# Kernel tuning notes

Hardware: AMD Instinct MI355X
Metric: run time of the kernel (lower is better)

Reference implementation:

```python
import jax, jax.numpy as jnp
import numpy as np

DEPTH = 4
H1 = 64
H2 = 16
NF = 5
L = 10.0
K = 4
DIM = 3
N = 2048
NK = N // 4
FEAT = 1 + 2 * NF * DIM  # r scalar + Nf (cos,sin) pairs of dim components


def _tn(k, shape, std=0.01):
    return jax.random.truncated_normal(k, -2.0, 2.0, shape, jnp.float32) * std


def setup_inputs() -> dict:
    key = jax.random.key(0)
    ks = jax.random.split(key, 16)
    comb0 = 3 * DIM + 3 * FEAT   # combine width at depth 0
    combd = 3 * H1 + 3 * H2      # combine width at later depths
    return {
        "sx": jax.random.uniform(ks[0], (N, DIM), jnp.float32) * L,
        "kpoints": jax.random.normal(ks[1], (2 * NK, DIM), jnp.float32),
        "we0": _tn(ks[2], (comb0, H1)), "be0": jnp.zeros((H1,), jnp.float32),
        "we_rest": _tn(ks[3], (DEPTH - 1, combd, H1)), "be_rest": jnp.zeros((DEPTH - 1, H1), jnp.float32),
        "wee0": _tn(ks[4], (FEAT, H2)), "bee0": jnp.zeros((H2,), jnp.float32),
        "wee_rest": _tn(ks[5], (DEPTH - 2, H2, H2)), "bee_rest": jnp.zeros((DEPTH - 2, H2), jnp.float32),
        "wep0": _tn(ks[6], (FEAT, H2)), "bep0": jnp.zeros((H2,), jnp.float32),
        "wep_rest": _tn(ks[7], (DEPTH - 2, H2, H2)), "bep_rest": jnp.zeros((DEPTH - 2, H2), jnp.float32),
        "orb_w_re": _tn(ks[8], (H1, H1)), "orb_w_im": _tn(ks[9], (H1, H1)),
        "orb_b_re": jnp.zeros((H1,), jnp.float32), "orb_b_im": jnp.zeros((H1,), jnp.float32),
        "w_det": _tn(ks[10], (K, H1, H1)),
        "bf_w": _tn(ks[11], (H1, DIM)),
        "mlp_w1": _tn(ks[12], (DIM, H1)), "mlp_b1": jnp.zeros((H1,), jnp.float32),
        "mlp_w2": _tn(ks[13], (H1, K * (NK - 1))), "mlp_b2": jnp.zeros((K * (NK - 1),), jnp.float32),
    }


def _fourier(rij, r):
    # interleaved [r, cos1, sin1, ..., cosNf, sinNf] like the original
    feats = [r[..., None]]
    for k in range(1, NF + 1):
        ang = (2.0 * np.pi * k / L) * rij
        feats.append(jnp.cos(ang))
        feats.append(jnp.sin(ang))
    return jnp.concatenate(feats, axis=-1)


def _combine(e, ee, ep):
    mm = e.shape[0]
    h = mm // 2
    g1a = jnp.broadcast_to(jnp.mean(e[:h], 0, keepdims=True), e.shape)
    g1b = jnp.broadcast_to(jnp.mean(e[h:], 0, keepdims=True), e.shape)
    g2a = jnp.mean(ee[:h], axis=0)
    g2b = jnp.mean(ee[h:], axis=0)
    g3 = jnp.mean(ep, axis=1)
    return jnp.concatenate([e, g1a, g1b, g2a, g2b, g3], axis=1)


def _forward(sx, kpoints, we0, be0, we_rest, be_rest, wee0, bee0, wee_rest, bee_rest,
             wep0, bep0, wep_rest, bep_rest, orb_w_re, orb_w_im, orb_b_re, orb_b_im,
             w_det, bf_w, mlp_w1, mlp_b1, mlp_w2, mlp_b2):
    n, dim = sx.shape
    m, m2 = n // 2, n // 4
    s, x = sx[:m], sx[m:]
    e = jnp.broadcast_to(kpoints[0][None, :], (m, dim))
    # electron-electron pairwise features (m,m,FEAT)
    rij = x[:, None, :] - x[None, :, :]
    eye = jnp.eye(m, dtype=x.dtype)
    r = jnp.linalg.norm(jnp.sin(np.pi * rij / L) + eye[..., None], axis=-1) * (1.0 - eye) * (L / np.pi)
    ee = _fourier(rij, r)
    # electron-proton pairwise features (m,m,FEAT)
    rij = x[:, None, :] - s[None, :, :]
    r = jnp.linalg.norm(jnp.sin(np.pi * rij / L), axis=-1) * (L / np.pi)
    ep = _fourier(rij, r)
    for d in range(DEPTH - 1):
        f = _combine(e, ee, ep)
        We, be = (we0, be0) if d == 0 else (we_rest[d - 1], be_rest[d - 1])
        Wee, bee = (wee0, bee0) if d == 0 else (wee_rest[d - 1], bee_rest[d - 1])
        Wep, bep = (wep0, bep0) if d == 0 else (wep_rest[d - 1], bep_rest[d - 1])
        e_u = jnp.tanh(f @ We + be)
        ee_u = jnp.tanh(ee @ Wee + bee)
        ep_u = jnp.tanh(ep @ Wep + bep)
        e, ee, ep = (e_u + e, ee_u + ee, ep_u + ep) if d > 0 else (e_u, ee_u, ep_u)
    f = _combine(e, ee, ep)
    e = jnp.tanh(f @ we_rest[-1] + be_rest[-1]) + e
    # complex orbitals and geminal pairing matrix phi: (K, m2, m2)
    orb = e.astype(jnp.complex64) @ (orb_w_re + 1j * orb_w_im) + (orb_b_re + 1j * orb_b_im)
    phi = jnp.einsum('ia,kab,jb->kij', orb[:m2], w_det.astype(jnp.complex64), orb[m2:]) + 1.0
    # backflow coordinates and plane-wave determinant factors
    z = e @ bf_w + x
    nk = kpoints.shape[0] // 2
    norm = 1.0 / L ** (dim / 2)
    D_up = norm * jnp.exp(1j * jnp.einsum('kd,id->ki', kpoints[:nk], z[:m2]))  # (nk, m2)
    D_dn = norm * jnp.exp(1j * jnp.einsum('kd,id->ki', kpoints[nk:], z[m2:]))  # (nk, m2)
    h = jnp.tanh(kpoints[0] @ mlp_w1 + mlp_b1)
    fdet = jax.nn.softplus(h @ mlp_w2 + mlp_b2).reshape(K, nk - 1)
    fdet = jnp.concatenate([jnp.ones((K, 1), fdet.dtype), fdet], axis=1)  # (K, nk)
    D = jnp.einsum('ai,ka,aj->kij', D_up, fdet.astype(D_up.dtype), jnp.conj(D_dn))
    # logdet_matmul: stable log of signed sum of K determinants
    phase, logabs = jnp.linalg.slogdet(D * phi)
    maxl = jnp.max(logabs)
    det = jnp.sum(phase * jnp.exp(logabs - maxl))
    return jnp.log(jnp.abs(det)) + maxl + jnp.log(det / jnp.abs(det))


def reference(sx, kpoints, we0, be0, we_rest, be_rest, wee0, bee0, wee_rest, bee_rest,
              wep0, bep0, wep_rest, bep_rest, orb_w_re, orb_w_im, orb_b_re, orb_b_im,
              w_det, bf_w, mlp_w1, mlp_b1, mlp_w2, mlp_b2):
    return _forward(sx, kpoints, we0, be0, we_rest, be_rest, wee0, bee0, wee_rest, bee_rest,
                    wep0, bep0, wep_rest, bep_rest, orb_w_re, orb_w_im, orb_b_re, orb_b_im,
                    w_det, bf_w, mlp_w1, mlp_b1, mlp_w2, mlp_b2)
```

## Files before the change

kernel.cpp:

```cpp
#include <hip/hip_runtime.h>

typedef unsigned int uint;
typedef unsigned short ushort;

#define M1 1024
#define MH 512
#define PI_F 3.14159265358979323846f
#define LBOX 10.0f
#define NB 32

__device__ __forceinline__ float bf2f(ushort h){ return __uint_as_float(((uint)h)<<16); }
__device__ __forceinline__ ushort f2bf(float f){ uint u = __float_as_uint(f); uint r = (u + 0x7fffu + ((u>>16)&1u))>>16; return (ushort)r; }
__device__ __forceinline__ float ftanh(float x){ float e = __expf(2.f*x); return 1.f - 2.f/(e+1.f); }
__device__ __forceinline__ float2 cmul(float2 a, float2 b){ return make_float2(a.x*b.x - a.y*b.y, a.x*b.y + a.y*b.x); }
__device__ __forceinline__ void cfma(float2& c, float2 a, float2 b){
  c.x = fmaf(a.x,b.x,fmaf(-a.y,b.y,c.x));
  c.y = fmaf(a.x,b.y,fmaf(a.y,b.x,c.y));
}

__device__ __forceinline__ void fourier31(float d0, float d1, float d2, bool diag, float f[31]){
  const float k1 = PI_F / LBOX;
  float s[3], c[3];
  __sincosf(k1*d0, &s[0], &c[0]);
  __sincosf(k1*d1, &s[1], &c[1]);
  __sincosf(k1*d2, &s[2], &c[2]);
  float r = diag ? 0.f : (LBOX/PI_F)*sqrtf(s[0]*s[0]+s[1]*s[1]+s[2]*s[2]);
  f[0] = r;
  float cb[3], sb[3], cc[3], sc[3];
  #pragma unroll
  for (int d=0; d<3; ++d){ cb[d] = 1.f - 2.f*s[d]*s[d]; sb[d] = 2.f*s[d]*c[d]; cc[d]=cb[d]; sc[d]=sb[d]; }
  #pragma unroll
  for (int k=0;k<5;++k){
    #pragma unroll
    for (int d=0; d<3; ++d){ f[1+6*k+d] = cc[d]; f[4+6*k+d] = sc[d]; }
    if (k<4){
      #pragma unroll
      for (int d=0; d<3; ++d){
        float nc = cc[d]*cb[d]-sc[d]*sb[d];
        float ns = sc[d]*cb[d]+cc[d]*sb[d];
        cc[d]=nc; sc[d]=ns;
      }
    }
  }
}

__global__ void k_init(float* __restrict__ p, int n, int* __restrict__ rowmap){
  int i = blockIdx.x*256 + threadIdx.x;
  if (i < 2048) rowmap[i] = i & 511;
  for (int q=i; q<n; q+=gridDim.x*256) p[q] = 0.f;
}

__global__ __launch_bounds__(256) void k_pair0(const float* __restrict__ sx, const float* __restrict__ W,
                                               const float* __restrict__ b, ushort* __restrict__ out, int is_ee,
                                               float* __restrict__ gA, float* __restrict__ gB,
                                               float* __restrict__ gH){
  int bx = blockIdx.x;
  int i = bx >> 2;
  int chunk = bx & 3;
  int j = (chunk << 8) + threadIdx.x;
  const float* xs = sx + 3*M1;
  float xi0 = xs[3*i], xi1 = xs[3*i+1], xi2 = xs[3*i+2];
  const float* oth = is_ee ? xs : sx;
  float y0 = oth[3*j], y1 = oth[3*j+1], y2 = oth[3*j+2];
  float f[31];
  fourier31(xi0-y0, xi1-y1, xi2-y2, is_ee && (i==j), f);
  float acc[16];
  #pragma unroll
  for (int o=0;o<16;++o) acc[o] = b[o];
  #pragma unroll
  for (int c=0;c<31;++c){ float fv = f[c];
    #pragma unroll
    for (int o=0;o<16;++o) acc[o] = fmaf(fv, W[c*16+o], acc[o]);
  }
  float hv[16];
  #pragma unroll
  for (int o=0;o<16;++o) hv[o] = ftanh(acc[o]);
  uint u[8];
  #pragma unroll
  for (int h=0;h<8;++h){
    u[h] = (uint)f2bf(hv[2*h]) | ((uint)f2bf(hv[2*h+1])<<16);
  }
  uint4* dst = (uint4*)(out + ((size_t)i*M1 + j)*16);
  dst[0] = make_uint4(u[0],u[1],u[2],u[3]);
  dst[1] = make_uint4(u[4],u[5],u[6],u[7]);
  __shared__ float buf[256*49];
  #pragma unroll
  for (int c=0;c<31;++c) buf[threadIdx.x*49+c] = f[c];
  #pragma unroll
  for (int c=0;c<16;++c) buf[threadIdx.x*49+31+c] = hv[c];
  __syncthreads();
  #pragma unroll
  for (int s=128; s>0; s>>=1){
    if (threadIdx.x < s){
      #pragma unroll
      for (int c=0;c<47;++c) buf[threadIdx.x*49+c] += buf[(threadIdx.x+s)*49+c];
    }
    __syncthreads();
  }
  if (threadIdx.x < 31){
    float* g = (is_ee && chunk >= 2) ? gB : gA;
    atomicAdd(&g[i*31+threadIdx.x], buf[threadIdx.x]);
  } else if (threadIdx.x < 47 && gH){
    atomicAdd(&gH[i*16 + (threadIdx.x-31)], buf[threadIdx.x]);
  }
}

__global__ __launch_bounds__(256) void k_pairU(ushort* __restrict__ ten, const float* __restrict__ W,
                                               const float* __restrict__ b, float* __restrict__ gOut){
  size_t base = ((size_t)blockIdx.x*256 + threadIdx.x)*16;
  uint4 a0 = ((uint4*)(ten+base))[0];
  uint4 a1 = ((uint4*)(ten+base))[1];
  uint uu[8] = {a0.x,a0.y,a0.z,a0.w,a1.x,a1.y,a1.z,a1.w};
  float v[16];
  #pragma unroll
  for (int h=0;h<8;++h){ v[2*h] = bf2f((ushort)(uu[h]&0xffffu)); v[2*h+1] = bf2f((ushort)(uu[h]>>16)); }
  float acc[16];
  #pragma unroll
  for (int o=0;o<16;++o) acc[o] = b[o];
  #pragma unroll
  for (int c=0;c<16;++c){ float fv = v[c];
    #pragma unroll
    for (int o=0;o<16;++o) acc[o] = fmaf(fv, W[c*16+o], acc[o]);
  }
  float nv[16];
  #pragma unroll
  for (int o=0;o<16;++o) nv[o] = ftanh(acc[o]) + v[o];
  uint w[8];
  #pragma unroll
  for (int h=0;h<8;++h){
    w[h] = (uint)f2bf(nv[2*h]) | ((uint)f2bf(nv[2*h+1])<<16);
  }
  ((uint4*)(ten+base))[0] = make_uint4(w[0],w[1],w[2],w[3]);
  ((uint4*)(ten+base))[1] = make_uint4(w[4],w[5],w[6],w[7]);
  __shared__ float buf[256*17];
  if (gOut){
    #pragma unroll
    for (int c=0;c<16;++c) buf[threadIdx.x*17+c] = nv[c];
    __syncthreads();
    #pragma unroll
    for (int s=128; s>0; s>>=1){
      if (threadIdx.x < s){
        #pragma unroll
        for (int c=0;c<16;++c) buf[threadIdx.x*17+c] += buf[(threadIdx.x+s)*17+c];
      }
      __syncthreads();
    }
    if (threadIdx.x < 16){
      int i = blockIdx.x >> 2;
      atomicAdd(&gOut[i*16 + threadIdx.x], buf[threadIdx.x]);
    }
  }
}

__global__ __launch_bounds__(256) void k_gee(const ushort* __restrict__ ten, float* __restrict__ gA, float* __restrict__ gB){
  int jb = blockIdx.x >> 3;
  int ic = blockIdx.x & 7;
  int jl = threadIdx.x & 63;
  int iq = threadIdx.x >> 6;
  int j = jb*64 + jl;
  float acc[16];
  #pragma unroll
  for (int c=0;c<16;++c) acc[c]=0.f;
  for (int s=0;s<32;++s){
    int i = ic*128 + iq + 4*s;
    const uint4* src = (const uint4*)(ten + ((size_t)i*M1 + j)*16);
    uint4 a0 = src[0], a1 = src[1];
    uint uu[8]={a0.x,a0.y,a0.z,a0.w,a1.x,a1.y,a1.z,a1.w};
    #pragma unroll
    for (int h=0;h<8;++h){ acc[2*h]+=bf2f((ushort)(uu[h]&0xffffu)); acc[2*h+1]+=bf2f((ushort)(uu[h]>>16)); }
  }
  __shared__ float red[4][64][16];
  #pragma unroll
  for (int c=0;c<16;++c) red[iq][jl][c]=acc[c];
  __syncthreads();
  if (iq==0){
    float* out = (ic<4)? gA : gB;
    #pragma unroll
    for (int c=0;c<16;++c){
      float t = red[0][jl][c]+red[1][jl][c]+red[2][jl][c]+red[3][jl][c];
      atomicAdd(&out[j*16+c], t);
    }
  }
}

__global__ __launch_bounds__(256) void k_e0(const float* __restrict__ kp, const float* __restrict__ g2a,
    const float* __restrict__ g2b, const float* __restrict__ g3, const float* __restrict__ W,
    const float* __restrict__ b, float* __restrict__ eout, float* __restrict__ g1out){
  int p = blockIdx.x*4 + (threadIdx.x>>6);
  int o = threadIdx.x & 63;
  float acc = b[o];
  #pragma unroll
  for (int d=0; d<3; ++d){
    acc = fmaf(kp[d], W[d*64+o] + W[(d+3)*64+o] + W[(d+6)*64+o], acc);
  }
  const float i512 = 1.f/512.f, i1024 = 1.f/1024.f;
  #pragma unroll
  for (int c=0;c<31;++c){
    float sg = (c!=0 && ((c-1)%6)>=3) ? -i512 : i512;
    acc = fmaf(g2a[p*31+c]*sg, W[(9+c)*64+o], acc);
  }
  #pragma unroll
  for (int c=0;c<31;++c){
    float sg = (c!=0 && ((c-1)%6)>=3) ? -i512 : i512;
    acc = fmaf(g2b[p*31+c]*sg, W[(40+c)*64+o], acc);
  }
  #pragma unroll
  for (int c=0;c<31;++c) acc = fmaf(g3[p*31+c]*i1024, W[(71+c)*64+o], acc);
  float v = ftanh(acc);
  eout[p*64+o] = v;
  atomicAdd(&g1out[(p<MH?0:64)+o], v);
}

__global__ __launch_bounds__(256) void k_eupd(const float* __restrict__ eprev, float* __restrict__ eout,
    const float* __restrict__ W, const float* __restrict__ b, const float* __restrict__ g1in,
    const float* __restrict__ g2a, const float* __restrict__ g2b, const float* __restrict__ g3,
    float* __restrict__ g1out){
  int p = blockIdx.x*4 + (threadIdx.x>>6);
  int o = threadIdx.x & 63;
  const float i512 = 1.f/512.f, i1024 = 1.f/1024.f;
  float acc = b[o];
  #pragma unroll 8
  for (int c=0;c<64;++c) acc = fmaf(eprev[p*64+c], W[c*64+o], acc);
  #pragma unroll 8
  for (int c=0;c<64;++c) acc = fmaf(g1in[c]*i512, W[(64+c)*64+o], acc);
  #pragma unroll 8
  for (int c=0;c<64;++c) acc = fmaf(g1in[64+c]*i512, W[(128+c)*64+o], acc);
  #pragma unroll
  for (int c=0;c<16;++c) acc = fmaf(g2a[p*16+c]*i512, W[(192+c)*64+o], acc);
  #pragma unroll
  for (int c=0;c<16;++c) acc = fmaf(g2b[p*16+c]*i512, W[(208+c)*64+o], acc);
  #pragma unroll
  for (int c=0;c<16;++c) acc = fmaf(g3[p*16+c]*i1024, W[(224+c)*64+o], acc);
  float v = ftanh(acc) + eprev[p*64+o];
  eout[p*64+o] = v;
  if (g1out) atomicAdd(&g1out[(p<MH?0:64)+o], v);
}

__global__ __launch_bounds__(256) void k_orbz(const float* __restrict__ e4, const float* __restrict__ Wre,
    const float* __restrict__ Wim, const float* __restrict__ bre, const float* __restrict__ bim,
    const float* __restrict__ bfw, const float* __restrict__ sx, float* __restrict__ ore,
    float* __restrict__ oim, float* __restrict__ z){
  int p = blockIdx.x*4 + (threadIdx.x>>6);
  int o = threadIdx.x & 63;
  float ar = bre[o], ai = bim[o];
  #pragma unroll 8
  for (int a=0;a<64;++a){ float ev = e4[p*64+a]; ar = fmaf(ev, Wre[a*64+o], ar); ai = fmaf(ev, Wim[a*64+o], ai); }
  ore[p*64+o]=ar; oim[p*64+o]=ai;
  if (o<3){
    float zz = sx[(M1+p)*3+o];
    for (int a=0;a<64;++a) zz = fmaf(e4[p*64+a], bfw[a*3+o], zz);
    z[p*3+o]=zz;
  }
}

__global__ __launch_bounds__(256) void k_fdet(const float* __restrict__ kp, const float* __restrict__ w1,
    const float* __restrict__ b1, const float* __restrict__ w2, const float* __restrict__ b2,
    float* __restrict__ fdet){
  __shared__ float hs[64];
  int tid = threadIdx.x;
  if (tid < 64){
    float acc = b1[tid];
    for (int d=0;d<3;++d) acc = fmaf(kp[d], w1[d*64+tid], acc);
    hs[tid] = ftanh(acc);
  }
  __syncthreads();
  int c = blockIdx.x*256 + tid;
  if (c < 2044){
    float acc = b2[c];
    #pragma unroll 8
    for (int o=0;o<64;++o) acc = fmaf(hs[o], w2[o*2044+c], acc);
    float sp = (acc > 20.f) ? acc : log1pf(__expf(acc));
    int kk = c / 511, idx = c % 511;
    fdet[kk*512 + 1 + idx] = sp;
  }
  if (blockIdx.x == 0 && tid < 4) fdet[tid*512] = 1.f;
}

__global__ __launch_bounds__(256) void k_uv(const float* __restrict__ kp, const float* __restrict__ z,
                                            float2* __restrict__ U, float2* __restrict__ V){
  int gid = blockIdx.x*256 + threadIdx.x;
  int sel = gid >> 18;
  int rem = gid & 262143;
  int a = rem >> 9;
  int col = rem & 511;
  const float nrm = 0.031622776601683794f;
  const float* kr = kp + (sel ? (512+a)*3 : a*3);
  const float* zr = z + (sel ? (512+col)*3 : col*3);
  float th = kr[0]*zr[0] + kr[1]*zr[1] + kr[2]*zr[2];
  float s, c; __sincosf(th, &s, &c);
  float2 v = make_float2(nrm*c, nrm*s);
  if (sel) V[a*512+col] = v; else U[a*512+col] = v;
}

__global__ __launch_bounds__(256) void k_T(const float* __restrict__ ore, const float* __restrict__ oim,
                                           const float* __restrict__ wdet, float2* __restrict__ T){
  int k = blockIdx.x >> 7;
  int iblk = blockIdx.x & 127;
  int i = iblk*4 + (threadIdx.x>>6);
  int bc = threadIdx.x & 63;
  __shared__ float wd[4096];
  for (int t = threadIdx.x; t < 4096; t += 256) wd[t] = wdet[k*4096 + t];
  __syncthreads();
  float ar=0.f, ai=0.f;
  #pragma unroll 8
  for (int a=0;a<64;++a){
    float w = wd[a*64+bc];
    ar = fmaf(ore[i*64+a], w, ar);
    ai = fmaf(oim[i*64+a], w, ai);
  }
  T[((size_t)k*512 + i)*64 + bc] = make_float2(ar, ai);
}

__global__ __launch_bounds__(256) void k_M(const float2* __restrict__ U, const float2* __restrict__ V,
    const float* __restrict__ fdet, const float2* __restrict__ T, const float* __restrict__ ore,
    const float* __restrict__ oim, float2* __restrict__ Mb){
  __shared__ float2 As[16*66];
  __shared__ float2 Bs[16*66];
  int k = blockIdx.z;
  int ib = blockIdx.y * 64, jb = blockIdx.x * 64;
  int tid = threadIdx.x;
  int ti = (tid >> 4) * 4;
  int tj = (tid & 15) * 4;
  const float* fk = fdet + k*512;
  float2 acc[4][4];
  #pragma unroll
  for (int a=0;a<4;++a){
    #pragma unroll
    for (int b=0;b<4;++b) acc[a][b] = make_float2(0.f,0.f);
  }
  for (int a0=0; a0<512; a0+=16){
    #pragma unroll
    for (int s=0;s<4;++s){
      int t = tid + s*256;
      int aa = t >> 6, il = t & 63;
      int a = a0 + aa;
      float fv = fk[a];
      float2 u = U[a*512 + ib + il];
      As[aa*66+il] = make_float2(u.x*fv, u.y*fv);
      float2 v = V[a*512 + jb + il];
      Bs[aa*66+il] = make_float2(v.x, -v.y);
    }
    __syncthreads();
    #pragma unroll
    for (int aa=0;aa<16;++aa){
      float2 Av[4], Bv[4];
      #pragma unroll
      for (int q=0;q<4;++q){ Av[q] = As[aa*66+ti+q]; Bv[q] = Bs[aa*66+tj+q]; }
      #pragma unroll
      for (int qi=0;qi<4;++qi){
        #pragma unroll
        for (int qj=0;qj<4;++qj) cfma(acc[qi][qj], Av[qi], Bv[qj]);
      }
    }
    __syncthreads();
  }
  float2 ph[4][4];
  #pragma unroll
  for (int a=0;a<4;++a){
    #pragma unroll
    for (int b=0;b<4;++b) ph[a][b] = make_float2(1.f,0.f);
  }
  for (int b0=0; b0<64; b0+=16){
    #pragma unroll
    for (int s=0;s<4;++s){
      int t = tid + s*256;
      int aa = t >> 6, il = t & 63;
      As[aa*66+il] = T[((size_t)k*512 + ib + il)*64 + b0 + aa];
      int oidx = (512 + jb + il)*64 + b0 + aa;
      Bs[aa*66+il] = make_float2(ore[oidx], oim[oidx]);
    }
    __syncthreads();
    #pragma unroll
    for (int aa=0;aa<16;++aa){
      float2 Av[4], Bv[4];
      #pragma unroll
      for (int q=0;q<4;++q){ Av[q] = As[aa*66+ti+q]; Bv[q] = Bs[aa*66+tj+q]; }
      #pragma unroll
      for (int qi=0;qi<4;++qi){
        #pragma unroll
        for (int qj=0;qj<4;++qj) cfma(ph[qi][qj], Av[qi], Bv[qj]);
      }
    }
    __syncthreads();
  }
  #pragma unroll
  for (int qi=0;qi<4;++qi){
    size_t ro = ((size_t)k*512 + ib + ti + qi)*512 + jb + tj;
    #pragma unroll
    for (int qj=0;qj<4;++qj) Mb[ro+qj] = cmul(acc[qi][qj], ph[qi][qj]);
  }
}

__global__ __launch_bounds__(512)
void k_panel(float2* __restrict__ Mb, float2* __restrict__ LinvG,
             int* __restrict__ rowmap, int* __restrict__ swapc, int col0){
  int k = blockIdx.x;
  float2* Mk = Mb + (size_t)k*512*512;
  int R = 512 - col0;
  int R64 = R < 64 ? R : 64;
  int rl = threadIdx.x;
  bool active = rl < R;
  int wv = rl >> 6;
  __shared__ float2 mir[64*33];
  __shared__ float2 Us[NB*33];
  __shared__ float2 dinv[NB];
  __shared__ float2 Ls[NB*NB];
  __shared__ float2 Yv[NB*NB];
  __shared__ int winslot[NB];
  __shared__ int newposS[64];
  int rm_orig = active ? rowmap[k*512 + col0 + rl] : 0;
  float2 X[NB];
  if (rl >= 64 && active){
    const float4* rp = (const float4*)(Mk + (size_t)rm_orig*512 + col0);
    #pragma unroll
    for (int q=0;q<NB/2;++q){ float4 v = rp[q]; X[2*q]=make_float2(v.x,v.y); X[2*q+1]=make_float2(v.z,v.w); }
  }
  if (wv == 0){
    if (rl < R64){
      const float4* rp = (const float4*)(Mk + (size_t)rm_orig*512 + col0);
      #pragma unroll
      for (int q=0;q<NB/2;++q){
        float4 v = rp[q];
        mir[rl*33+2*q]   = make_float2(v.x,v.y);
        mir[rl*33+2*q+1] = make_float2(v.z,v.w);
      }
    }
    bool done = false;
    int winpos = 0;
    for (int cc=0; cc<NB; ++cc){
      bool cand = (rl < R64) && !done;
      float2 cv = make_float2(0.f,0.f);
      if (cand) cv = mir[rl*33+cc];
      float val = cand ? fmaf(cv.x,cv.x,cv.y*cv.y) : -1.f;
      int idx = rl;
      #pragma unroll
      for (int off=32; off>0; off>>=1){
        float ov = __shfl_xor(val, off);
        int   oi = __shfl_xor(idx, off);
        if (ov > val || (ov == val && oi < idx)){ val = ov; idx = oi; }
      }
      int p = idx;
      if (rl == 0) winslot[cc] = p;
      if (rl == p){ done = true; winpos = cc; }
      float2 dg = mir[p*33+cc];
      float dn = 1.f/fmaf(dg.x,dg.x,dg.y*dg.y);
      float2 inv = make_float2(dg.x*dn, -dg.y*dn);
      if (cand && rl != p){
        float2 l = cmul(cv, inv);
        mir[rl*33+cc] = l;
        for (int j=cc+1; j<NB; ++j){
          float2 pr = mir[p*33+j];
          float2 xv = mir[rl*33+j];
          xv.x = fmaf(-l.x, pr.x, fmaf( l.y, pr.y, xv.x));
          xv.y = fmaf(-l.x, pr.y, fmaf(-l.y, pr.x, xv.y));
          mir[rl*33+j] = xv;
        }
      }
    }
    unsigned long long nwmask = __ballot(rl < R64 && !done);
    int np = 0;
    if (rl < R64){
      np = done ? winpos : (NB + (int)__popcll(nwmask & ((1ull<<rl)-1ull)));
      newposS[rl] = np;
      rowmap[k*512 + col0 + np] = rm_orig;
      float4* wp = (float4*)(Mk + (size_t)rm_orig*512 + col0);
      #pragma unroll
      for (int q=0;q<NB/2;++q){
        float2 a = mir[rl*33+2*q], bq = mir[rl*33+2*q+1];
        wp[q] = make_float4(a.x,a.y,bq.x,bq.y);
      }
    }
    {
      int cnt = 0;
      for (int t=0;t<R64;++t){
        int nt = newposS[t];
        if (rl < R64 && t > rl && nt < np) cnt++;
      }
      #pragma unroll
      for (int off=32; off>0; off>>=1) cnt += __shfl_xor(cnt, off);
      if (rl == 0) swapc[k] += cnt;
    }
    if (rl < NB){
      int ws = winslot[rl];
      #pragma unroll
      for (int j=0;j<NB;++j){
        float2 v = mir[ws*33+j];
        Us[rl*33+j] = v;
        float2 lv;
        if      (j <  rl) lv = v;
        else if (j == rl) lv = make_float2(1.f,0.f);
        else              lv = make_float2(0.f,0.f);
        Ls[rl*NB+j] = lv;
      }
      float2 d = Us[rl*33+rl];
      float dn = 1.f/fmaf(d.x,d.x,d.y*d.y);
      dinv[rl] = make_float2(d.x*dn, -d.y*dn);
    }
  }
  __syncthreads();
  if (rl >= 64 && active){
    #pragma unroll
    for (int j=0;j<NB;++j){
      float2 t = X[j];
      #pragma unroll
      for (int q=0;q<NB;++q){
        if (q < j){
          float2 u = Us[q*33+j];
          t.x = fmaf(-X[q].x, u.x, fmaf( X[q].y, u.y, t.x));
          t.y = fmaf(-X[q].x, u.y, fmaf(-X[q].y, u.x, t.y));
        }
      }
      X[j] = cmul(t, dinv[j]);
    }
    float4* wp = (float4*)(Mk + (size_t)rm_orig*512 + col0);
    #pragma unroll
    for (int q=0;q<NB/2;++q) wp[q] = make_float4(X[2*q].x,X[2*q].y,X[2*q+1].x,X[2*q+1].y);
  }
  if (rl < NB){
    for (int i=0;i<NB;++i){
      float2 acc = (i==rl)? make_float2(1.f,0.f) : make_float2(0.f,0.f);
      for (int q=rl; q<i; ++q){
        float2 lv = Ls[i*NB+q];
        float2 yv = Yv[q*NB+rl];
        acc.x = fmaf(-lv.x, yv.x, fmaf( lv.y, yv.y, acc.x));
        acc.y = fmaf(-lv.x, yv.y, fmaf(-lv.y, yv.x, acc.y));
      }
      Yv[i*NB+rl] = acc;
    }
  }
  __syncthreads();
  {
    float4* dst = (float4*)(LinvG + (size_t)k*(NB*NB));
    const float4* src = (const float4*)Yv;
    for (int q=rl; q<NB*NB/2; q+=blockDim.x) dst[q] = src[q];
  }
}

__global__ __launch_bounds__(256) void k_gemm(float2* __restrict__ Mb, const float2* __restrict__ LinvG,
                                              const int* __restrict__ rowmap, int col0){
  int k = blockIdx.z;
  float2* Mk = Mb + (size_t)k*512*512;
  int e0 = col0 + NB;
  int r0 = e0 + blockIdx.x*32;
  int j0c = e0 + blockIdx.y*32;
  int tid = threadIdx.x;
  int jl = tid & 31, rg = tid >> 5;
  __shared__ float2 As[NB*33];
  __shared__ float2 Bs[NB*33];
  __shared__ float2 Av[NB*33];
  __shared__ float2 Li[NB*NB];
  __shared__ int prA[32];
  __shared__ int prB[NB];
  if (tid < 32) prA[tid] = rowmap[k*512 + r0 + tid];
  else if (tid < 64) prB[tid-32] = rowmap[k*512 + col0 + (tid-32)];
  {
    const float4* src = (const float4*)(LinvG + (size_t)k*(NB*NB));
    float4* dst = (float4*)Li;
    for (int q=tid; q<NB*NB/2; q+=256) dst[q] = src[q];
  }
  __syncthreads();
  #pragma unroll
  for (int s=0;s<4;++s){
    int a = rg + 8*s;
    Av[a*33 + jl] = Mk[(size_t)prB[a]*512 + j0c + jl];
  }
  for (int t=tid; t<1024; t+=256){
    int rl = t >> 5, kk = t & 31;
    As[kk*33+rl] = Mk[(size_t)prA[rl]*512 + col0 + kk];
  }
  __syncthreads();
  #pragma unroll
  for (int s=0;s<4;++s){
    int m = rg + 8*s;
    float2 acc = make_float2(0.f,0.f);
    #pragma unroll 8
    for (int a=0;a<NB;++a) cfma(acc, Li[m*NB+a], Av[a*33+jl]);
    Bs[m*33+jl] = acc;
  }
  __syncthreads();
  int i0 = (tid >> 4)*2, j0 = (tid & 15)*2;
  float2 a00={0,0},a01={0,0},a10={0,0},a11={0,0};
  #pragma unroll 16
  for (int kk=0;kk<NB;++kk){
    float2 A0 = As[kk*33+i0], A1 = As[kk*33+i0+1];
    float2 B0 = Bs[kk*33+j0], B1 = Bs[kk*33+j0+1];
    cfma(a00,A0,B0); cfma(a01,A0,B1); cfma(a10,A1,B0); cfma(a11,A1,B1);
  }
  size_t ro0 = (size_t)prA[i0]*512 + j0c + j0;
  size_t ro1 = (size_t)prA[i0+1]*512 + j0c + j0;
  float2 c0 = Mk[ro0];   c0.x-=a00.x; c0.y-=a00.y; Mk[ro0]=c0;
  float2 c1 = Mk[ro0+1]; c1.x-=a01.x; c1.y-=a01.y; Mk[ro0+1]=c1;
  float2 c2 = Mk[ro1];   c2.x-=a10.x; c2.y-=a10.y; Mk[ro1]=c2;
  float2 c3 = Mk[ro1+1]; c3.x-=a11.x; c3.y-=a11.y; Mk[ro1+1]=c3;
}

__global__ void k_det(const float2* __restrict__ Mb, const int* __restrict__ rowmap,
                      const int* __restrict__ swapc, float* __restrict__ out, int out_size){
  int tid = threadIdx.x;
  int k = tid >> 6, lane = tid & 63;
  const float2* Mk = Mb + (size_t)k*512*512;
  double la = 0.0, ang = 0.0;
  for (int q=0;q<8;++q){
    int i = lane*8 + q;
    int pr = rowmap[k*512 + i];
    float2 u = Mk[(size_t)pr*512+i];
    double re = (double)u.x, im = (double)u.y;
    la += 0.5*log(re*re + im*im);
    ang += atan2(im, re);
  }
  #pragma unroll
  for (int off=32; off>0; off>>=1){
    la += __shfl_down(la, off);
    ang += __shfl_down(ang, off);
  }
  __shared__ double las[4], angs[4];
  if (lane==0){
    las[k] = la;
    angs[k] = ang + 3.14159265358979323846*(double)(swapc[k] & 1);
  }
  __syncthreads();
  if (tid==0){
    double mx = las[0];
    for (int q=1;q<4;++q) mx = fmax(mx, las[q]);
    double sre=0.0, sim=0.0;
    for (int q=0;q<4;++q){
      double w = exp(las[q]-mx);
      sre += w*cos(angs[q]);
      sim += w*sin(angs[q]);
    }
    double mag = sqrt(sre*sre+sim*sim);
    out[0] = (float)(log(mag)+mx);
    if (out_size > 1) out[1] = (float)atan2(sim, sre);
    for (int q=2;q<out_size;++q) out[q] = 0.f;
  }
}

extern "C" void kernel_launch(void* const* d_in, const int* in_sizes, int n_in,
                              void* d_out, int out_size, void* d_ws, size_t ws_size,
                              hipStream_t stream){
  const float* sx   = (const float*)d_in[0];
  const float* kp   = (const float*)d_in[1];
  const float* we0  = (const float*)d_in[2];
  const float* be0  = (const float*)d_in[3];
  const float* weR  = (const float*)d_in[4];
  const float* beR  = (const float*)d_in[5];
  const float* wee0 = (const float*)d_in[6];
  const float* bee0 = (const float*)d_in[7];
  const float* weeR = (const float*)d_in[8];
  const float* beeR = (const float*)d_in[9];
  const float* wep0 = (const float*)d_in[10];
  const float* bep0 = (const float*)d_in[11];
  const float* wepR = (const float*)d_in[12];
  const float* bepR = (const float*)d_in[13];
  const float* owre = (const float*)d_in[14];
  const float* owim = (const float*)d_in[15];
  const float* obre = (const float*)d_in[16];
  const float* obim = (const float*)d_in[17];
  const float* wdet = (const float*)d_in[18];
  const float* bfw  = (const float*)d_in[19];
  const float* mw1  = (const float*)d_in[20];
  const float* mb1  = (const float*)d_in[21];
  const float* mw2  = (const float*)d_in[22];
  const float* mb2  = (const float*)d_in[23];

  char* ws = (char*)d_ws;
  size_t off = 0;
  auto alloc = [&](size_t bytes)->char*{
    char* p = ws + off;
    off = (off + bytes + 255) & ~(size_t)255;
    return p;
  };
  ushort* ee   = (ushort*)alloc(33554432);
  ushort* ep   = (ushort*)alloc(33554432);
  float2* Mb   = (float2*)alloc(8388608);
  float2* U    = (float2*)alloc(2097152);
  float2* V    = (float2*)alloc(2097152);
  float2* T    = (float2*)alloc(1048576);
  float*  eS   = (float*)alloc(1048576);
  float*  ore  = (float*)alloc(262144);
  float*  oim  = (float*)alloc(262144);
  float*  z    = (float*)alloc(12288);
  float*  fdet = (float*)alloc(8192);
  float2* Linv = (float2*)alloc(131072);
  int*    rowmap = (int*)alloc(8192);
  char*   zst  = ws + off;
  float*  g2a0 = (float*)alloc(126976);
  float*  g2b0 = (float*)alloc(126976);
  float*  g30  = (float*)alloc(126976);
  float*  geeA = (float*)alloc(196608);
  float*  geeB = (float*)alloc(196608);
  float*  gep  = (float*)alloc(196608);
  float*  g1s  = (float*)alloc(1536);
  int*    swpc = (int*)alloc(16);
  int zn = (int)(((char*)(swpc+4) - zst)/4);

  float* e1 = eS;           float* e2 = eS + 65536;
  float* e3 = eS + 131072;  float* e4 = eS + 196608;
  float* geeA1 = geeA;      float* geeA2 = geeA+16384; float* geeA3 = geeA+32768;
  float* geeB1 = geeB;      float* geeB2 = geeB+16384; float* geeB3 = geeB+32768;
  float* gep1  = gep;       float* gep2  = gep+16384;  float* gep3  = gep+32768;
  float* g1s1 = g1s; float* g1s2 = g1s+128; float* g1s3 = g1s+256;

  k_init<<<256,256,0,stream>>>((float*)zst, zn, rowmap);
  k_pair0<<<4096,256,0,stream>>>(sx, wee0, bee0, ee, 1, g2a0, g2b0, nullptr);
  k_pair0<<<4096,256,0,stream>>>(sx, wep0, bep0, ep, 0, g30, g30, gep1);
  k_e0<<<256,256,0,stream>>>(kp, g2a0, g2b0, g30, we0, be0, e1, g1s1);
  k_gee<<<128,256,0,stream>>>(ee, geeA1, geeB1);
  k_eupd<<<256,256,0,stream>>>(e1, e2, weR, beR, g1s1, geeA1, geeB1, gep1, g1s2);
  k_pairU<<<4096,256,0,stream>>>(ee, weeR, beeR, nullptr);
  k_pairU<<<4096,256,0,stream>>>(ep, wepR, bepR, gep2);
  k_gee<<<128,256,0,stream>>>(ee, geeA2, geeB2);
  k_eupd<<<256,256,0,stream>>>(e2, e3, weR+240*64, beR+64, g1s2, geeA2, geeB2, gep2, g1s3);
  k_pairU<<<4096,256,0,stream>>>(ee, weeR+256, beeR+16, nullptr);
  k_pairU<<<4096,256,0,stream>>>(ep, wepR+256, bepR+16, gep3);
  k_gee<<<128,256,0,stream>>>(ee, geeA3, geeB3);
  k_eupd<<<256,256,0,stream>>>(e3, e4, weR+2*240*64, beR+128, g1s3, geeA3, geeB3, gep3, nullptr);
  k_orbz<<<256,256,0,stream>>>(e4, owre, owim, obre, obim, bfw, sx, ore, oim, z);
  k_fdet<<<8,256,0,stream>>>(kp, mw1, mb1, mw2, mb2, fdet);
  k_uv<<<2048,256,0,stream>>>(kp, z, U, V);
  k_T<<<512,256,0,stream>>>(ore, oim, wdet, T);
  k_M<<<dim3(8,8,4),256,0,stream>>>(U, V, fdet, T, ore, oim, Mb);
  for (int tpan=0;tpan<16;++tpan){
    int col0 = tpan*NB;
    int R = 512 - col0;
    int Rpad = (R + 63) & ~63;
    k_panel<<<4, Rpad, 0, stream>>>(Mb, Linv, rowmap, swpc, col0);
    if (tpan < 15){
      int nch = 15 - tpan;
      k_gemm<<<dim3(nch,nch,4),256,0,stream>>>(Mb, Linv, rowmap, col0);
    }
  }
  k_det<<<1,256,0,stream>>>(Mb, rowmap, swpc, (float*)d_out, out_size);
  (void)in_sizes; (void)n_in; (void)ws_size;
}
```

Measured before the change: 1.894 ms.

## Retile k_M into 32x32 output tiles with 2x2 per-thread work

The M-matrix build kernel moves from 64x64 tiles with 4x4 outputs per thread over 256 blocks to 32x32 tiles with 2x2 outputs per thread over 1024 blocks. The phase GEMM now stages the full T and orbital slices into shared memory once instead of in four chunks. The aim is to fill more of the GPU's compute units on this small launch, at the cost of less register reuse and more global traffic per output.

```diff
diff --git a/kernel.cpp b/kernel.cpp
--- a/kernel.cpp
+++ b/kernel.cpp
@@ -314,81 +314,57 @@
 __global__ __launch_bounds__(256) void k_M(const float2* __restrict__ U, const float2* __restrict__ V,
     const float* __restrict__ fdet, const float2* __restrict__ T, const float* __restrict__ ore,
     const float* __restrict__ oim, float2* __restrict__ Mb){
-  __shared__ float2 As[16*66];
-  __shared__ float2 Bs[16*66];
-  int k = blockIdx.z;
-  int ib = blockIdx.y * 64, jb = blockIdx.x * 64;
-  int tid = threadIdx.x;
-  int ti = (tid >> 4) * 4;
-  int tj = (tid & 15) * 4;
+  __shared__ float2 sm[4160];
+  int k = blockIdx.x >> 8;
+  int ty = (blockIdx.x >> 4) & 15;
+  int tx = blockIdx.x & 15;
+  int ib = ty*32, jb = tx*32;
+  int i0 = (threadIdx.x >> 4)*2;
+  int j0 = threadIdx.x & 15;
   const float* fk = fdet + k*512;
-  float2 acc[4][4];
-  #pragma unroll
-  for (int a=0;a<4;++a){
-    #pragma unroll
-    for (int b=0;b<4;++b) acc[a][b] = make_float2(0.f,0.f);
-  }
+  float2 a00={0,0},a01={0,0},a10={0,0},a11={0,0};
+  float2* As = sm;
+  float2* Bs = sm + 512;
   for (int a0=0; a0<512; a0+=16){
-    #pragma unroll
-    for (int s=0;s<4;++s){
-      int t = tid + s*256;
-      int aa = t >> 6, il = t & 63;
+    for (int t = threadIdx.x; t < 512; t += 256){
+      int aa = t >> 5, il = t & 31;
       int a = a0 + aa;
       float fv = fk[a];
       float2 u = U[a*512 + ib + il];
-      As[aa*66+il] = make_float2(u.x*fv, u.y*fv);
+      As[t] = make_float2(u.x*fv, u.y*fv);
       float2 v = V[a*512 + jb + il];
-      Bs[aa*66+il] = make_float2(v.x, -v.y);
+      Bs[t] = make_float2(v.x, -v.y);
     }
     __syncthreads();
     #pragma unroll
-    for (int aa=0;aa<16;++aa){
-      float2 Av[4], Bv[4];
-      #pragma unroll
-      for (int q=0;q<4;++q){ Av[q] = As[aa*66+ti+q]; Bv[q] = Bs[aa*66+tj+q]; }
-      #pragma unroll
-      for (int qi=0;qi<4;++qi){
-        #pragma unroll
-        for (int qj=0;qj<4;++qj) cfma(acc[qi][qj], Av[qi], Bv[qj]);
-      }
+    for (int aa=0; aa<16; ++aa){
+      float2 A0 = As[aa*32+i0], A1 = As[aa*32+i0+1];
+      float2 B0 = Bs[aa*32+j0], B1 = Bs[aa*32+j0+16];
+      cfma(a00,A0,B0); cfma(a01,A0,B1); cfma(a10,A1,B0); cfma(a11,A1,B1);
     }
     __syncthreads();
   }
-  float2 ph[4][4];
-  #pragma unroll
-  for (int a=0;a<4;++a){
-    #pragma unroll
-    for (int b=0;b<4;++b) ph[a][b] = make_float2(1.f,0.f);
-  }
-  for (int b0=0; b0<64; b0+=16){
-    #pragma unroll
-    for (int s=0;s<4;++s){
-      int t = tid + s*256;
-      int aa = t >> 6, il = t & 63;
-      As[aa*66+il] = T[((size_t)k*512 + ib + il)*64 + b0 + aa];
-      int oidx = (512 + jb + il)*64 + b0 + aa;
-      Bs[aa*66+il] = make_float2(ore[oidx], oim[oidx]);
-    }
-    __syncthreads();
-    #pragma unroll
-    for (int aa=0;aa<16;++aa){
-      float2 Av[4], Bv[4];
-      #pragma unroll
-      for (int q=0;q<4;++q){ Av[q] = As[aa*66+ti+q]; Bv[q] = Bs[aa*66+tj+q]; }
-      #pragma unroll
-      for (int qi=0;qi<4;++qi){
-        #pragma unroll
-        for (int qj=0;qj<4;++qj) cfma(ph[qi][qj], Av[qi], Bv[qj]);
-      }
-    }
-    __syncthreads();
-  }
-  #pragma unroll
-  for (int qi=0;qi<4;++qi){
-    size_t ro = ((size_t)k*512 + ib + ti + qi)*512 + jb + tj;
-    #pragma unroll
-    for (int qj=0;qj<4;++qj) Mb[ro+qj] = cmul(acc[qi][qj], ph[qi][qj]);
-  }
+  float2* Ts = sm;
+  float2* Od = sm + 2080;
+  for (int t = threadIdx.x; t < 2048; t += 256){
+    int il = t >> 6, bc = t & 63;
+    Ts[il*65+bc] = T[((size_t)k*512 + ib + il)*64 + bc];
+    int oidx = (512 + jb + il)*64 + bc;
+    Od[il*65+bc] = make_float2(ore[oidx], oim[oidx]);
+  }
+  __syncthreads();
+  float2 p00={1,0},p01={1,0},p10={1,0},p11={1,0};
+  #pragma unroll 8
+  for (int bb=0; bb<64; ++bb){
+    float2 T0 = Ts[i0*65+bb], T1 = Ts[(i0+1)*65+bb];
+    float2 O0 = Od[j0*65+bb], O1 = Od[(j0+16)*65+bb];
+    cfma(p00,T0,O0); cfma(p01,T0,O1); cfma(p10,T1,O0); cfma(p11,T1,O1);
+  }
+  size_t base = ((size_t)k*512 + ib + i0)*512 + jb;
+  Mb[base+j0]        = cmul(a00, p00);
+  Mb[base+j0+16]     = cmul(a01, p01);
+  Mb[base+512+j0]    = cmul(a10, p10);
+  Mb[base+512+j0+16] = cmul(a11, p11);
 }
 
 __global__ __launch_bounds__(512)
@@ -719,7 +695,7 @@
   k_fdet<<<8,256,0,stream>>>(kp, mw1, mb1, mw2, mb2, fdet);
   k_uv<<<2048,256,0,stream>>>(kp, z, U, V);
   k_T<<<512,256,0,stream>>>(ore, oim, wdet, T);
-  k_M<<<dim3(8,8,4),256,0,stream>>>(U, V, fdet, T, ore, oim, Mb);
+  k_M<<<1024,256,0,stream>>>(U, V, fdet, T, ore, oim, Mb);
   for (int tpan=0;tpan<16;++tpan){
     int col0 = tpan*NB;
     int R = 512 - col0;
```

After: 1.852 ms. 1.02x faster.
